# Performance work log

Measured on AMD Instinct MI355X. Metric: run time of the kernel, lower is better.

The kernel has to match this reference:

```python
import jax, jax.numpy as jnp
import numpy as np

B, S, HID = 1, 2048, 4096
NH, NKV, HD = 32, 8, 128
EPS = 1e-6
SCALE = HD ** -0.5


def _rope_cos_sin(seq_len, head_dim, base=1000000.0):
    inv_freq = 1.0 / (base ** (np.arange(0, head_dim, 2, dtype=np.float32) / head_dim))
    t = np.arange(seq_len, dtype=np.float32)
    freqs = np.outer(t, inv_freq)                      # [S, HD/2]
    emb = np.concatenate([freqs, freqs], axis=-1)       # [S, HD]
    return jnp.asarray(np.cos(emb))[None], jnp.asarray(np.sin(emb))[None]  # [1,S,HD]


def setup_inputs() -> dict:
    key = jax.random.key(0)
    ks = jax.random.split(key, 8)
    cos, sin = _rope_cos_sin(S, HD)
    inp = {
        "hidden_states": jax.random.normal(ks[0], (B, S, HID), jnp.float32),
        "cos": jnp.broadcast_to(cos, (B, S, HD)),
        "sin": jnp.broadcast_to(sin, (B, S, HD)),
        "Wq": jax.random.normal(ks[1], (NH * HD, HID), jnp.float32) * 0.02,
        "Wk": jax.random.normal(ks[2], (NKV * HD, HID), jnp.float32) * 0.02,
        "Wv": jax.random.normal(ks[3], (NKV * HD, HID), jnp.float32) * 0.02,
        "Wo": jax.random.normal(ks[4], (HID, NH * HD), jnp.float32) * 0.02,
        "q_norm_w": jnp.ones((HD,), jnp.float32),
        "k_norm_w": jnp.ones((HD,), jnp.float32),
    }
    return inp


def _rmsnorm(x, w, eps=EPS):
    var = jnp.mean(jnp.square(x), axis=-1, keepdims=True)
    return x * jax.lax.rsqrt(var + eps) * w


def _rotate_half(x):
    x1, x2 = jnp.split(x, 2, axis=-1)
    return jnp.concatenate([-x2, x1], axis=-1)


def _apply_rope(x, cos, sin):
    # x: [b,s,n,d]; cos/sin: [b,s,d] -> unsqueeze head dim (dim=2)
    c = cos[:, :, None, :]
    s = sin[:, :, None, :]
    return x * c + _rotate_half(x) * s


def reference(hidden_states, cos, sin, Wq, Wk, Wv, Wo, q_norm_w, k_norm_w):
    b, s, _ = hidden_states.shape
    q = (hidden_states @ Wq.T).reshape(b, s, NH, HD)
    k = (hidden_states @ Wk.T).reshape(b, s, NKV, HD)
    v = (hidden_states @ Wv.T).reshape(b, s, NKV, HD)
    # per-head RMSNorm on q and k
    q = _rmsnorm(q, q_norm_w)
    k = _rmsnorm(k, k_norm_w)
    # RoPE
    q = _apply_rope(q, cos, sin)
    k = _apply_rope(k, cos, sin)
    # GQA: expand kv heads to match query heads (group size = NH // NKV)
    g = NH // NKV
    k = jnp.repeat(k, g, axis=2)  # [b,s,NH,d]
    v = jnp.repeat(v, g, axis=2)
    # causal SDPA, layout bsnd
    scores = jnp.einsum("bqhd,bkhd->bhqk", q, k) * SCALE
    causal = jnp.tril(jnp.ones((s, s), dtype=bool))
    scores = jnp.where(causal[None, None], scores, jnp.finfo(scores.dtype).min)
    probs = jax.nn.softmax(scores, axis=-1)
    attn = jnp.einsum("bhqk,bkhd->bqhd", probs, v).reshape(b, s, NH * HD)
    return attn @ Wo.T
```

## Files before the change

### kernel.cpp

```cpp
#include <hip/hip_runtime.h>
#include <hip/hip_bf16.h>
#include <stdint.h>

#define S_LEN 2048
#define HIDD  4096
#define NH    32
#define NKV   8
#define HD    128
#define NQKV  6144
#define ATT_SCALE 0.08838834764831845f
#define LOG2E 1.4426950408889634f

typedef unsigned short u16;
typedef __attribute__((ext_vector_type(8))) short short8;
typedef __attribute__((ext_vector_type(4))) float f32x4;

__device__ __forceinline__ unsigned f2bfbits(float f){
  union{float f; unsigned u;} v; v.f = f;
  return (v.u + 0x7FFFu + ((v.u>>16)&1u)) >> 16;
}
__device__ __forceinline__ float bf2f(u16 b){
  union{unsigned u; float f;} v; v.u = ((unsigned)b)<<16;
  return v.f;
}
__device__ __forceinline__ unsigned packbf(float a, float b){
  return f2bfbits(a) | (f2bfbits(b)<<16);
}
__device__ __forceinline__ unsigned cvtpk(float lo, float hi){
  unsigned r;
  asm("v_cvt_pk_bf16_f32 %0, %1, %2" : "=v"(r) : "v"(lo), "v"(hi));
  return r;
}

#define GLOAD16(g, l) __builtin_amdgcn_global_load_lds( \
    (__attribute__((address_space(1))) void*)(g), \
    (__attribute__((address_space(3))) void*)(l), 16, 0, 0)

#define VMWAIT(n) asm volatile("s_waitcnt vmcnt(" #n ")" ::: "memory")
#define SCHED0() __builtin_amdgcn_sched_barrier(0)

__global__ __launch_bounds__(256) void cvt_all(const float* __restrict__ hs,
                                               const float* __restrict__ Wq,
                                               const float* __restrict__ Wk,
                                               const float* __restrict__ Wv,
                                               u16* __restrict__ Xb,
                                               u16* __restrict__ WQKV){
  const float* src; u16* dst; int n8;
  switch (blockIdx.y){
    case 0: src = hs; dst = Xb;                        n8 = S_LEN*HIDD/8;    break;
    case 1: src = Wq; dst = WQKV;                      n8 = NH*HD*HIDD/8;    break;
    case 2: src = Wk; dst = WQKV + (size_t)NH*HD*HIDD; n8 = NKV*HD*HIDD/8;   break;
    default:src = Wv; dst = WQKV + (size_t)(NH+NKV)*HD*HIDD; n8 = NKV*HD*HIDD/8; break;
  }
  int i = blockIdx.x*256 + threadIdx.x;
  if (i >= n8) return;
  const float4* p = (const float4*)src;
  float4 a = p[2*i], b = p[2*i+1];
  union { unsigned u[4]; short8 s; } o;
  o.u[0] = packbf(a.x, a.y); o.u[1] = packbf(a.z, a.w);
  o.u[2] = packbf(b.x, b.y); o.u[3] = packbf(b.z, b.w);
  *(short8*)(dst + (size_t)i*8) = o.s;
}

__global__ __launch_bounds__(256) void cvt_bf16(const float* __restrict__ in,
                                                u16* __restrict__ out, int n8){
  int i = blockIdx.x*256 + threadIdx.x;
  if (i >= n8) return;
  const float4* p = (const float4*)in;
  float4 a = p[2*i], b = p[2*i+1];
  union { unsigned u[4]; short8 s; } o;
  o.u[0] = packbf(a.x, a.y); o.u[1] = packbf(a.z, a.w);
  o.u[2] = packbf(b.x, b.y); o.u[3] = packbf(b.z, b.w);
  *(short8*)(out + (size_t)i*8) = o.s;
}

template<int BM, int BN, typename OT>
__global__ __launch_bounds__(512) void gemm_4ph(const u16* __restrict__ A,
                                                const u16* __restrict__ B,
                                                OT* __restrict__ C,
                                                int N, int K, int nbx){
  constexpr int MREP = BM/32;
  constexpr int NF   = BN/64;
  constexpr int AH   = BM/128;
  constexpr int ASZ  = BM*64;
  __shared__ __align__(16) char lds[4*ASZ + 65536];

  const int tid = threadIdx.x;
  const int w = tid>>6, lane = tid&63, ln = lane&15, g = lane>>4;
  const int wm = w>>2, wn = w&3;
  const int swz5 = ((ln>>3)&1)<<5;

  const int nwg = gridDim.x, flat = blockIdx.x;
  const int wg = (flat&7)*(nwg>>3) + (flat>>3);
  const int by = wg/nbx, bx = wg - by*nbx;
  const int m0 = by*BM, n0 = bx*BN;

  const int rs   = ((tid>>6)<<4) + ((tid&63)>>2);
  const int ksrc = ((tid&3)<<3) ^ (((tid>>5)&1)<<4);
  const u16* srcA[AH];
  #pragma unroll
  for (int h=0;h<AH;h++) srcA[h] = A + (size_t)(m0 + h*128 + rs)*K + ksrc;
  const u16* srcB[2];
  #pragma unroll
  for (int h=0;h<2;h++)  srcB[h] = B + (size_t)(n0 + h*128 + rs)*K + ksrc;

  #define AREG(bf,kh) (lds + ((bf)*2 + (kh))*ASZ)
  #define BREG(bf,kh) (lds + 4*ASZ + ((bf)*2 + (kh))*16384)

  #define STAGEPT(t, kh, bf) { const int off_ = (t)*64 + (kh)*32;                 \
    _Pragma("unroll") for (int h=0;h<AH;h++)                                      \
      GLOAD16(srcA[h]+off_, AREG(bf,kh) + h*8192 + w*1024);                       \
    _Pragma("unroll") for (int h=0;h<2;h++)                                       \
      GLOAD16(srcB[h]+off_, BREG(bf,kh) + h*8192 + w*1024); }

  f32x4 acc[MREP][NF];
  #pragma unroll
  for (int m=0;m<MREP;m++)
    #pragma unroll
    for (int n=0;n<NF;n++) acc[m][n] = (f32x4){0.f,0.f,0.f,0.f};
  short8 a0_[MREP], b0_[NF], a1_[MREP], b1_[NF];

  #define READ_SET(aset, bset, bf, kh) {                                          \
    _Pragma("unroll") for (int n=0;n<NF;n++)                                      \
      bset[n] = *(const short8*)(BREG(bf,kh) + (wn*NF+n)*1024 + ln*64 + ((g*16)^swz5)); \
    _Pragma("unroll") for (int m=0;m<MREP;m++)                                    \
      aset[m] = *(const short8*)(AREG(bf,kh) + (wm*MREP+m)*1024 + ln*64 + ((g*16)^swz5)); }
  #define MFMA_SET(aset, bset) { __builtin_amdgcn_s_setprio(1);                   \
    _Pragma("unroll") for (int m=0;m<MREP;m++)                                    \
      _Pragma("unroll") for (int n=0;n<NF;n++)                                    \
        acc[m][n] = __builtin_amdgcn_mfma_f32_16x16x32_bf16(aset[m], bset[n], acc[m][n], 0,0,0); \
    __builtin_amdgcn_s_setprio(0); }
  #define BARR() __builtin_amdgcn_s_barrier()
  #define VMST() do{ if constexpr (AH==2) { VMWAIT(4); } else { VMWAIT(3); } }while(0)

  STAGEPT(0,0,0); STAGEPT(0,1,0); STAGEPT(1,0,1);
  VMWAIT(0); BARR(); SCHED0();
  READ_SET(a0_, b0_, 0, 0);

  const int NIT = K>>7;
  #pragma unroll 1
  for (int it=0; it<NIT; ++it){
    const bool last = (it == NIT-1);
    const int t0 = 2*it;
    READ_SET(a1_, b1_, 0, 1);
    STAGEPT(t0+1, 1, 1);
    MFMA_SET(a0_, b0_);
    SCHED0(); VMST(); BARR(); SCHED0();
    READ_SET(a0_, b0_, 1, 0);
    if (!last) STAGEPT(t0+2, 0, 0);
    MFMA_SET(a1_, b1_);
    SCHED0(); if (last) { VMWAIT(0); } else { VMST(); } BARR(); SCHED0();
    READ_SET(a1_, b1_, 1, 1);
    if (!last) STAGEPT(t0+2, 1, 0);
    MFMA_SET(a0_, b0_);
    SCHED0(); if (!last) { VMST(); } BARR(); SCHED0();
    if (!last){ READ_SET(a0_, b0_, 0, 0); STAGEPT(t0+3, 0, 1); }
    MFMA_SET(a1_, b1_);
    if (!last){ SCHED0(); VMST(); BARR(); SCHED0(); }
  }

  #pragma unroll
  for (int mi=0; mi<MREP; mi++)
    #pragma unroll
    for (int n=0; n<NF; n++)
      #pragma unroll
      for (int r=0;r<4;r++){
        int row = m0 + (wm*MREP+mi)*16 + g*4 + r;
        int col = n0 + wn*(NF*16) + n*16 + ln;
        if constexpr (__is_same(OT, u16))
          C[(size_t)row*N + col] = (u16)f2bfbits(acc[mi][n][r]);
        else
          C[(size_t)row*N + col] = acc[mi][n][r];
      }
  #undef AREG
  #undef BREG
  #undef STAGEPT
  #undef READ_SET
  #undef MFMA_SET
  #undef BARR
  #undef VMST
}

__global__ __launch_bounds__(256) void norm_rope(const u16* __restrict__ QKVb,
                                                 const float* __restrict__ cosb,
                                                 const float* __restrict__ sinb,
                                                 const float* __restrict__ qw,
                                                 const float* __restrict__ kw,
                                                 u16* __restrict__ Qn,
                                                 u16* __restrict__ Kn,
                                                 u16* __restrict__ Vt){
  int w = threadIdx.x>>6, lane = threadIdx.x&63;
  int row = blockIdx.x*4 + w;
  int s = row / 48, slot = row - s*48;
  const u16* src = QKVb + (size_t)s*NQKV + slot*HD;
  float x0 = bf2f(src[lane]), x1 = bf2f(src[lane+64]);
  if (slot < 40){
    float ss = x0*x0 + x1*x1;
    #pragma unroll
    for (int off=1; off<64; off<<=1) ss += __shfl_xor(ss, off, 64);
    float r = rsqrtf(ss*(1.0f/128.0f) + 1e-6f);
    const float* wgt = (slot < 32) ? qw : kw;
    float y0 = x0*r*wgt[lane], y1 = x1*r*wgt[lane+64];
    float c0 = cosb[(size_t)s*HD+lane], c1 = cosb[(size_t)s*HD+lane+64];
    float s0 = sinb[(size_t)s*HD+lane], s1 = sinb[(size_t)s*HD+lane+64];
    float o0 = y0*c0 - y1*s0;
    float o1 = y1*c1 + y0*s1;
    float sc = (slot < 32) ? (ATT_SCALE*LOG2E) : 1.0f;
    u16* dst = (slot < 32) ? (Qn + ((size_t)slot*S_LEN + s)*HD)
                           : (Kn + ((size_t)(slot-32)*S_LEN + s)*HD);
    dst[lane]    = (u16)f2bfbits(o0*sc);
    dst[lane+64] = (u16)f2bfbits(o1*sc);
  } else {
    int kvh = slot - 40;
    u16* dst = Vt + (size_t)kvh*HD*S_LEN + s;
    dst[(size_t)lane*S_LEN]      = (u16)f2bfbits(x0);
    dst[(size_t)(lane+64)*S_LEN] = (u16)f2bfbits(x1);
  }
}

__global__ __launch_bounds__(256) void flash_attn(const u16* __restrict__ Qn,
                                                  const u16* __restrict__ Kn,
                                                  const u16* __restrict__ Vt,
                                                  u16* __restrict__ O){
  __shared__ u16 Ks[2][64*128];
  __shared__ u16 Vs[2][128*64];

  const int h = blockIdx.y;
  const int w = threadIdx.x>>6, lane = threadIdx.x&63, ln = lane&15, g = lane>>4;
  const int kvh = h>>2;
  const u16* Qh = Qn + (size_t)h*S_LEN*HD;
  const u16* Kh = Kn + (size_t)kvh*S_LEN*HD;
  const u16* Vh = Vt + (size_t)kvh*HD*S_LEN;

  const int krow_w = w*4 + g;
  const int ksw    = ((krow_w)&7)<<4;
  const int kcol   = ((ln*16) ^ ksw) >> 1;
  const int vrow_w = w*8 + (lane>>3);
  const int vsw    = ((lane>>3)&7)<<4;
  const int vcol   = (((lane&7)*16) ^ vsw) >> 1;

  #define STAGE_K(bufi, t) { \
    int kv0_ = (t)*64; \
    _Pragma("unroll") \
    for (int p=0;p<4;p++){ \
      const u16* ga = Kh + (size_t)(kv0_ + p*16 + krow_w)*HD + kcol; \
      GLOAD16(ga, (char*)&Ks[bufi][0] + p*4096 + w*1024); \
    } \
  }
  #define STAGE_V(bufi, t) { \
    int kv0_ = (t)*64; \
    _Pragma("unroll") \
    for (int p=0;p<4;p++){ \
      const u16* gv = Vh + (size_t)(p*32 + vrow_w)*S_LEN + kv0_ + vcol; \
      GLOAD16(gv, (char*)&Vs[bufi][0] + p*4096 + w*1024); \
    } \
  }
  #define QKT(dst, buf) { \
    _Pragma("unroll") for (int mt=0; mt<4; mt++){ \
      short8 kf[4]; \
      _Pragma("unroll") for (int c=0;c<4;c++) \
        kf[c] = *(const short8*)((const char*)&Ks[buf][0] \
                    + (mt*16+ln)*256 + ((c*64 + g*16) ^ ((ln&7)<<4))); \
      f32x4 qacc = (f32x4){0.f,0.f,0.f,0.f}; \
      __builtin_amdgcn_s_setprio(1); \
      _Pragma("unroll") for (int c=0;c<4;c++) \
        qacc = __builtin_amdgcn_mfma_f32_16x16x32_bf16(kf[c], qf[c], qacc, 0,0,0); \
      __builtin_amdgcn_s_setprio(0); \
      dst[mt] = qacc; \
    } }

  #define TILE_BODY(i, SC, SN) { \
    VMWAIT(0); \
    __builtin_amdgcn_s_barrier(); \
    if ((i)+1 < nt){ \
      QKT(SN, ((i)+1)&1); \
      if ((i)+2 < nt) STAGE_K(((i)+2)&1, (i)+2); \
      STAGE_V(((i)+1)&1, (i)+1); \
    } \
    const int kv0 = (i)*64; \
    float p[4][4]; \
    float mtile = -1e30f; \
    if ((i) < qb){ \
      _Pragma("unroll") for (int mt=0; mt<4; mt++) \
        _Pragma("unroll") for (int r=0;r<4;r++){ \
          p[mt][r] = SC[mt][r]; \
          mtile = fmaxf(mtile, SC[mt][r]); \
        } \
    } else { \
      _Pragma("unroll") for (int mt=0; mt<4; mt++) \
        _Pragma("unroll") for (int r=0;r<4;r++){ \
          int kv = kv0 + mt*16 + 4*g + r; \
          float sv = (kv <= qrow) ? SC[mt][r] : -1e30f; \
          p[mt][r] = sv; \
          mtile = fmaxf(mtile, sv); \
        } \
    } \
    mtile = fmaxf(mtile, __shfl_xor(mtile, 16, 64)); \
    mtile = fmaxf(mtile, __shfl_xor(mtile, 32, 64)); \
    bool defer = __all(mtile <= m_run + 11.5416f); \
    float m_new = defer ? m_run : fmaxf(m_run, mtile); \
    float l_tile = 0.f; \
    _Pragma("unroll") for (int mt=0; mt<4; mt++) \
      _Pragma("unroll") for (int r=0;r<4;r++){ \
        float e = exp2f(p[mt][r] - m_new); \
        p[mt][r] = e; \
        l_tile += e; \
      } \
    l_tile += __shfl_xor(l_tile, 16, 64); \
    l_tile += __shfl_xor(l_tile, 32, 64); \
    if (defer){ \
      l_run += l_tile; \
    } else { \
      float alpha = exp2f(m_run - m_new); \
      l_run = l_run*alpha + l_tile; \
      m_run = m_new; \
      _Pragma("unroll") for (int dt=0;dt<8;dt++) ot[dt] *= alpha; \
    } \
    short8 pf[2]; \
    _Pragma("unroll") for (int ks2=0; ks2<2; ks2++){ \
      unsigned pk00 = cvtpk(p[2*ks2  ][0], p[2*ks2  ][1]); \
      unsigned pk01 = cvtpk(p[2*ks2  ][2], p[2*ks2  ][3]); \
      unsigned pk10 = cvtpk(p[2*ks2+1][0], p[2*ks2+1][1]); \
      unsigned pk11 = cvtpk(p[2*ks2+1][2], p[2*ks2+1][3]); \
      int src0 = (((2*g  )&3)<<4) | ln; \
      int src1 = (((2*g+1)&3)<<4) | ln; \
      unsigned t00 = (unsigned)__shfl((int)pk00, src0, 64); \
      unsigned t10 = (unsigned)__shfl((int)pk10, src0, 64); \
      unsigned t01 = (unsigned)__shfl((int)pk01, src0, 64); \
      unsigned t11 = (unsigned)__shfl((int)pk11, src0, 64); \
      unsigned u00 = (unsigned)__shfl((int)pk00, src1, 64); \
      unsigned u10 = (unsigned)__shfl((int)pk10, src1, 64); \
      unsigned u01 = (unsigned)__shfl((int)pk01, src1, 64); \
      unsigned u11 = (unsigned)__shfl((int)pk11, src1, 64); \
      bool hiv = (g >= 2); \
      union { unsigned u[4]; short8 s; } pw; \
      pw.u[0] = hiv ? t10 : t00; \
      pw.u[1] = hiv ? t11 : t01; \
      pw.u[2] = hiv ? u10 : u00; \
      pw.u[3] = hiv ? u11 : u01; \
      pf[ks2] = pw.s; \
    } \
    _Pragma("unroll") for (int dt=0;dt<8;dt++){ \
      short8 vf[2]; \
      _Pragma("unroll") for (int ks2=0; ks2<2; ks2++) \
        vf[ks2] = *(const short8*)((const char*)&Vs[(i)&1][0] \
                    + (dt*16+ln)*128 + ((ks2*64 + g*16) ^ ((ln&7)<<4))); \
      __builtin_amdgcn_s_setprio(1); \
      _Pragma("unroll") for (int ks2=0; ks2<2; ks2++) \
        ot[dt] = __builtin_amdgcn_mfma_f32_16x16x32_bf16(vf[ks2], pf[ks2], ot[dt], 0,0,0); \
      __builtin_amdgcn_s_setprio(0); \
    } \
  }

  #pragma unroll 1
  for (int ph=0; ph<2; ph++){
    const int qb = ph ? (31 - blockIdx.x) : blockIdx.x;
    const int q0 = qb*64;
    const int qrow = q0 + w*16 + ln;

    short8 qf[4];
    #pragma unroll
    for (int c=0;c<4;c++)
      qf[c] = *(const short8*)(Qh + (size_t)qrow*HD + c*32 + g*8);

    f32x4 ot[8];
    #pragma unroll
    for (int dt=0;dt<8;dt++) ot[dt] = (f32x4){0.f,0.f,0.f,0.f};
    float m_run = -1e30f, l_run = 0.f;

    const int nt = qb + 1;

    STAGE_K(0, 0); STAGE_V(0, 0);
    if (nt > 1) STAGE_K(1, 1);
    VMWAIT(0);
    __builtin_amdgcn_s_barrier();

    f32x4 stA[4], stB[4];
    QKT(stA, 0);

    #pragma unroll 1
    for (int i=0; i<nt; i+=2){
      TILE_BODY(i, stA, stB);
      if (i+1 < nt) TILE_BODY(i+1, stB, stA);
    }
    __syncthreads();

    float inv = 1.0f / l_run;
    u16* orow = O + (size_t)qrow*(NH*HD) + h*HD;
    #pragma unroll
    for (int dt=0;dt<8;dt++){
      #pragma unroll
      for (int rr=0; rr<4; rr+=2){
        unsigned pkd = cvtpk(ot[dt][rr]*inv, ot[dt][rr+1]*inv);
        *(unsigned*)(orow + dt*16 + g*4 + rr) = pkd;
      }
    }
  }
  #undef STAGE_K
  #undef STAGE_V
  #undef QKT
  #undef TILE_BODY
}

extern "C" void kernel_launch(void* const* d_in, const int* in_sizes, int n_in,
                              void* d_out, int out_size, void* d_ws, size_t ws_size,
                              hipStream_t stream){
  (void)in_sizes; (void)n_in; (void)out_size; (void)ws_size;
  const float* hs   = (const float*)d_in[0];
  const float* cosb = (const float*)d_in[1];
  const float* sinb = (const float*)d_in[2];
  const float* Wq   = (const float*)d_in[3];
  const float* Wk   = (const float*)d_in[4];
  const float* Wv   = (const float*)d_in[5];
  const float* Wo   = (const float*)d_in[6];
  const float* qw   = (const float*)d_in[7];
  const float* kw   = (const float*)d_in[8];
  float* out = (float*)d_out;

  char* ws = (char*)d_ws;
  u16*   Xb    = (u16*)  (ws);
  u16*   WQKV  = (u16*)  (ws + 16777216);
  u16*   QKVb  = (u16*)  (ws + 67108864);
  u16*   attnB = (u16*)  (ws + 94371840);
  u16*   Qn    = (u16*)  (ws + 117440512);
  u16*   Kn    = (u16*)  (ws + 134217728);
  u16*   Vt    = (u16*)  (ws + 138412032);
  u16*   Wob   = WQKV;

  cvt_all<<<dim3(8192, 4), 256, 0, stream>>>(hs, Wq, Wk, Wv, Xb, WQKV);
  gemm_4ph<256,192,u16><<<256, 512, 0, stream>>>(Xb, WQKV, QKVb, NQKV, HIDD, NQKV/192);
  norm_rope<<<(S_LEN*48)/4, 256, 0, stream>>>(QKVb, cosb, sinb, qw, kw, Qn, Kn, Vt);
  cvt_bf16<<<(HIDD*NH*HD/8)/256, 256, 0, stream>>>(Wo, Wob, HIDD*NH*HD/8);
  flash_attn<<<dim3(16, NH), 256, 0, stream>>>(Qn, Kn, Vt, attnB);
  gemm_4ph<128,256,float><<<256, 512, 0, stream>>>(attnB, Wob, out, HIDD, HIDD, HIDD/256);
}
```

Baseline: 330.7 us.

## Restructure GEMM to 4-wave 256-thread blocks with smaller tiles and single register set

Both GEMMs now use 256-thread workgroups in a 2x2 wave layout. Tiles shrink to 128x192 for the QKV projection and 128x128 for the output projection, which doubles the grid to 512 blocks. The double-buffered register prefetch (two A/B operand sets) becomes a single set that is read right before each MFMA cluster, and the vmcnt wait counts are retuned for the new load counts. The aim is better CU occupancy and load balance across the GPU. In exchange, each block reuses data less and LDS read latency is no longer hidden behind the previous MFMA block.

```diff
diff --git a/kernel.cpp b/kernel.cpp
--- a/kernel.cpp
+++ b/kernel.cpp
@@ -75,19 +75,21 @@
 }
 
 template<int BM, int BN, typename OT>
-__global__ __launch_bounds__(512) void gemm_4ph(const u16* __restrict__ A,
+__global__ __launch_bounds__(256) void gemm_4ph(const u16* __restrict__ A,
                                                 const u16* __restrict__ B,
                                                 OT* __restrict__ C,
                                                 int N, int K, int nbx){
   constexpr int MREP = BM/32;
-  constexpr int NF   = BN/64;
-  constexpr int AH   = BM/128;
+  constexpr int NF   = BN/32;
+  constexpr int AL   = BM/64;
+  constexpr int BL   = BN/64;
   constexpr int ASZ  = BM*64;
-  __shared__ __align__(16) char lds[4*ASZ + 65536];
+  constexpr int BSZ  = BN*64;
+  __shared__ __align__(16) char lds[4*ASZ + 4*BSZ];
 
   const int tid = threadIdx.x;
   const int w = tid>>6, lane = tid&63, ln = lane&15, g = lane>>4;
-  const int wm = w>>2, wn = w&3;
+  const int wm = w>>1, wn = w&1;
   const int swz5 = ((ln>>3)&1)<<5;
 
   const int nwg = gridDim.x, flat = blockIdx.x;
@@ -97,66 +99,62 @@
 
   const int rs   = ((tid>>6)<<4) + ((tid&63)>>2);
   const int ksrc = ((tid&3)<<3) ^ (((tid>>5)&1)<<4);
-  const u16* srcA[AH];
+  const u16* srcA[AL];
   #pragma unroll
-  for (int h=0;h<AH;h++) srcA[h] = A + (size_t)(m0 + h*128 + rs)*K + ksrc;
-  const u16* srcB[2];
+  for (int j=0;j<AL;j++) srcA[j] = A + (size_t)(m0 + 64*j + rs)*K + ksrc;
+  const u16* srcB[BL];
   #pragma unroll
-  for (int h=0;h<2;h++)  srcB[h] = B + (size_t)(n0 + h*128 + rs)*K + ksrc;
+  for (int j=0;j<BL;j++) srcB[j] = B + (size_t)(n0 + 64*j + rs)*K + ksrc;
 
   #define AREG(bf,kh) (lds + ((bf)*2 + (kh))*ASZ)
-  #define BREG(bf,kh) (lds + 4*ASZ + ((bf)*2 + (kh))*16384)
+  #define BREG(bf,kh) (lds + 4*ASZ + ((bf)*2 + (kh))*BSZ)
 
   #define STAGEPT(t, kh, bf) { const int off_ = (t)*64 + (kh)*32;                 \
-    _Pragma("unroll") for (int h=0;h<AH;h++)                                      \
-      GLOAD16(srcA[h]+off_, AREG(bf,kh) + h*8192 + w*1024);                       \
-    _Pragma("unroll") for (int h=0;h<2;h++)                                       \
-      GLOAD16(srcB[h]+off_, BREG(bf,kh) + h*8192 + w*1024); }
+    _Pragma("unroll") for (int j=0;j<AL;j++)                                      \
+      GLOAD16(srcA[j]+off_, AREG(bf,kh) + (4*j+w)*1024);                          \
+    _Pragma("unroll") for (int j=0;j<BL;j++)                                      \
+      GLOAD16(srcB[j]+off_, BREG(bf,kh) + (4*j+w)*1024); }
 
   f32x4 acc[MREP][NF];
   #pragma unroll
   for (int m=0;m<MREP;m++)
     #pragma unroll
     for (int n=0;n<NF;n++) acc[m][n] = (f32x4){0.f,0.f,0.f,0.f};
-  short8 a0_[MREP], b0_[NF], a1_[MREP], b1_[NF];
-
-  #define READ_SET(aset, bset, bf, kh) {                                          \
-    _Pragma("unroll") for (int n=0;n<NF;n++)                                      \
-      bset[n] = *(const short8*)(BREG(bf,kh) + (wn*NF+n)*1024 + ln*64 + ((g*16)^swz5)); \
-    _Pragma("unroll") for (int m=0;m<MREP;m++)                                    \
-      aset[m] = *(const short8*)(AREG(bf,kh) + (wm*MREP+m)*1024 + ln*64 + ((g*16)^swz5)); }
-  #define MFMA_SET(aset, bset) { __builtin_amdgcn_s_setprio(1);                   \
+  short8 a_[MREP], b_[NF];
+
+  #define READA(bf,kh) { _Pragma("unroll") for (int m=0;m<MREP;m++)               \
+    a_[m] = *(const short8*)(AREG(bf,kh) + (wm*MREP+m)*1024 + ln*64 + ((g*16)^swz5)); }
+  #define READB(bf,kh) { _Pragma("unroll") for (int n=0;n<NF;n++)                 \
+    b_[n] = *(const short8*)(BREG(bf,kh) + (wn*NF+n)*1024 + ln*64 + ((g*16)^swz5)); }
+  #define MFMACLU() { __builtin_amdgcn_s_setprio(1);                              \
     _Pragma("unroll") for (int m=0;m<MREP;m++)                                    \
       _Pragma("unroll") for (int n=0;n<NF;n++)                                    \
-        acc[m][n] = __builtin_amdgcn_mfma_f32_16x16x32_bf16(aset[m], bset[n], acc[m][n], 0,0,0); \
+        acc[m][n] = __builtin_amdgcn_mfma_f32_16x16x32_bf16(a_[m], b_[n], acc[m][n], 0,0,0); \
     __builtin_amdgcn_s_setprio(0); }
   #define BARR() __builtin_amdgcn_s_barrier()
-  #define VMST() do{ if constexpr (AH==2) { VMWAIT(4); } else { VMWAIT(3); } }while(0)
+  #define VM2LP() do{ if constexpr (AL+BL==5) { VMWAIT(10); } else { VMWAIT(8); } }while(0)
+  #define VM1LP() do{ if constexpr (AL+BL==5) { VMWAIT(5); }  else { VMWAIT(4); } }while(0)
 
   STAGEPT(0,0,0); STAGEPT(0,1,0); STAGEPT(1,0,1);
   VMWAIT(0); BARR(); SCHED0();
-  READ_SET(a0_, b0_, 0, 0);
 
   const int NIT = K>>7;
   #pragma unroll 1
   for (int it=0; it<NIT; ++it){
     const bool last = (it == NIT-1);
     const int t0 = 2*it;
-    READ_SET(a1_, b1_, 0, 1);
-    STAGEPT(t0+1, 1, 1);
-    MFMA_SET(a0_, b0_);
-    SCHED0(); VMST(); BARR(); SCHED0();
-    READ_SET(a0_, b0_, 1, 0);
-    if (!last) STAGEPT(t0+2, 0, 0);
-    MFMA_SET(a1_, b1_);
-    SCHED0(); if (last) { VMWAIT(0); } else { VMST(); } BARR(); SCHED0();
-    READ_SET(a1_, b1_, 1, 1);
-    if (!last) STAGEPT(t0+2, 1, 0);
-    MFMA_SET(a0_, b0_);
-    SCHED0(); if (!last) { VMST(); } BARR(); SCHED0();
-    if (!last){ READ_SET(a0_, b0_, 0, 0); STAGEPT(t0+3, 0, 1); }
-    MFMA_SET(a1_, b1_);
-    if (!last){ SCHED0(); VMST(); BARR(); SCHED0(); }
+    READB(0,0); READA(0,0); STAGEPT(t0+1, 1, 1);
+    MFMACLU();
+    SCHED0(); VM2LP(); BARR(); SCHED0();
+    READB(0,1); READA(0,1); if (!last) STAGEPT(t0+2, 0, 0);
+    MFMACLU();
+    SCHED0(); if (last) { VM1LP(); } else { VM2LP(); } BARR(); SCHED0();
+    READB(1,0); READA(1,0); if (!last) STAGEPT(t0+2, 1, 0);
+    MFMACLU();
+    SCHED0(); if (last) { VMWAIT(0); } else { VM2LP(); } BARR(); SCHED0();
+    READB(1,1); READA(1,1); if (!last) STAGEPT(t0+3, 0, 1);
+    MFMACLU();
+    SCHED0(); if (!last) { VM2LP(); } BARR(); SCHED0();
   }
 
   #pragma unroll
@@ -166,7 +164,7 @@
       #pragma unroll
       for (int r=0;r<4;r++){
         int row = m0 + (wm*MREP+mi)*16 + g*4 + r;
-        int col = n0 + wn*(NF*16) + n*16 + ln;
+        int col = n0 + (wn*NF+n)*16 + ln;
         if constexpr (__is_same(OT, u16))
           C[(size_t)row*N + col] = (u16)f2bfbits(acc[mi][n][r]);
         else
@@ -175,10 +173,12 @@
   #undef AREG
   #undef BREG
   #undef STAGEPT
-  #undef READ_SET
-  #undef MFMA_SET
+  #undef READA
+  #undef READB
+  #undef MFMACLU
   #undef BARR
-  #undef VMST
+  #undef VM2LP
+  #undef VM1LP
 }
 
 __global__ __launch_bounds__(256) void norm_rope(const u16* __restrict__ QKVb,
@@ -428,9 +428,9 @@
   u16*   Wob   = WQKV;
 
   cvt_all<<<dim3(8192, 4), 256, 0, stream>>>(hs, Wq, Wk, Wv, Xb, WQKV);
-  gemm_4ph<256,192,u16><<<256, 512, 0, stream>>>(Xb, WQKV, QKVb, NQKV, HIDD, NQKV/192);
+  gemm_4ph<128,192,u16><<<512, 256, 0, stream>>>(Xb, WQKV, QKVb, NQKV, HIDD, NQKV/192);
   norm_rope<<<(S_LEN*48)/4, 256, 0, stream>>>(QKVb, cosb, sinb, qw, kw, Qn, Kn, Vt);
   cvt_bf16<<<(HIDD*NH*HD/8)/256, 256, 0, stream>>>(Wo, Wob, HIDD*NH*HD/8);
   flash_attn<<<dim3(16, NH), 256, 0, stream>>>(Qn, Kn, Vt, attnB);
-  gemm_4ph<128,256,float><<<256, 512, 0, stream>>>(attnB, Wob, out, HIDD, HIDD, HIDD/256);
-}
+  gemm_4ph<128,128,float><<<512, 256, 0, stream>>>(attnB, Wob, out, HIDD, HIDD, HIDD/128);
+}
```

After: 374.7 us. 1.13x slower.

## Fuse QK RMSNorm and RoPE into QKV GEMM epilogue, merge Wo conversion

Applied to the files above, without the earlier changes.

Replaces the QKV GEMM plus separate norm_rope kernel with a dedicated GEMM using 128x384 tiles, so each tile covers three whole heads. The epilogue stages the tile in LDS, then applies per-head RMSNorm, RoPE and the query scale, and writes Q, K and transposed V directly. This removes the intermediate QKV buffer round trip and one kernel launch. The Wo fp32-to-bf16 conversion is folded into cvt_all as a fifth grid row, which drops another launch. The new GEMM tile shape and its serial per-row epilogue (shuffle reductions, strided V-transpose stores) may be less efficient than the previous tuned GEMM configuration.

```diff
diff --git a/kernel.cpp b/kernel.cpp
--- a/kernel.cpp
+++ b/kernel.cpp
@@ -43,14 +43,17 @@
                                                const float* __restrict__ Wq,
                                                const float* __restrict__ Wk,
                                                const float* __restrict__ Wv,
+                                               const float* __restrict__ Wo,
                                                u16* __restrict__ Xb,
-                                               u16* __restrict__ WQKV){
+                                               u16* __restrict__ WQKV,
+                                               u16* __restrict__ Wob){
   const float* src; u16* dst; int n8;
   switch (blockIdx.y){
     case 0: src = hs; dst = Xb;                        n8 = S_LEN*HIDD/8;    break;
     case 1: src = Wq; dst = WQKV;                      n8 = NH*HD*HIDD/8;    break;
     case 2: src = Wk; dst = WQKV + (size_t)NH*HD*HIDD; n8 = NKV*HD*HIDD/8;   break;
-    default:src = Wv; dst = WQKV + (size_t)(NH+NKV)*HD*HIDD; n8 = NKV*HD*HIDD/8; break;
+    case 3: src = Wv; dst = WQKV + (size_t)(NH+NKV)*HD*HIDD; n8 = NKV*HD*HIDD/8; break;
+    default:src = Wo; dst = Wob;                       n8 = HIDD*NH*HD/8;    break;
   }
   int i = blockIdx.x*256 + threadIdx.x;
   if (i >= n8) return;
@@ -62,16 +65,142 @@
   *(short8*)(dst + (size_t)i*8) = o.s;
 }
 
-__global__ __launch_bounds__(256) void cvt_bf16(const float* __restrict__ in,
-                                                u16* __restrict__ out, int n8){
-  int i = blockIdx.x*256 + threadIdx.x;
-  if (i >= n8) return;
-  const float4* p = (const float4*)in;
-  float4 a = p[2*i], b = p[2*i+1];
-  union { unsigned u[4]; short8 s; } o;
-  o.u[0] = packbf(a.x, a.y); o.u[1] = packbf(a.z, a.w);
-  o.u[2] = packbf(b.x, b.y); o.u[3] = packbf(b.z, b.w);
-  *(short8*)(out + (size_t)i*8) = o.s;
+__global__ __launch_bounds__(512) void gemm1_fused(const u16* __restrict__ A,
+                                                   const u16* __restrict__ B,
+                                                   const float* __restrict__ cosb,
+                                                   const float* __restrict__ sinb,
+                                                   const float* __restrict__ qw,
+                                                   const float* __restrict__ kw,
+                                                   u16* __restrict__ Qn,
+                                                   u16* __restrict__ Kn,
+                                                   u16* __restrict__ Vt){
+  __shared__ __align__(16) char lds[131072];
+
+  const int tid = threadIdx.x;
+  const int w = tid>>6, lane = tid&63, ln = lane&15, g = lane>>4;
+  const int wm = w>>2, wn = w&3;
+  const int swz5 = ((ln>>3)&1)<<5;
+  const int K = HIDD;
+
+  const int nwg = gridDim.x, flat = blockIdx.x;
+  const int wg = (flat&7)*(nwg>>3) + (flat>>3);
+  const int by = wg>>4, bx = wg&15;
+  const int m0 = by*128, n0 = bx*384;
+
+  const int rs   = ((tid>>6)<<4) + ((tid&63)>>2);
+  const int ksrc = ((tid&3)<<3) ^ (((tid>>5)&1)<<4);
+  const u16* srcA0 = A + (size_t)(m0 + rs)*K + ksrc;
+  const u16* srcB[3];
+  #pragma unroll
+  for (int j=0;j<3;j++) srcB[j] = B + (size_t)(n0 + 128*j + rs)*K + ksrc;
+
+  #define G1_AREG(bf,kh) (lds + ((bf)*2 + (kh))*8192)
+  #define G1_BREG(bf,kh) (lds + 32768 + ((bf)*2 + (kh))*24576)
+
+  #define G1_STAGE(T, kh, bf) { const int off_ = (T)*64 + (kh)*32;                \
+    GLOAD16(srcA0 + off_, G1_AREG(bf,kh) + w*1024);                               \
+    _Pragma("unroll") for (int j=0;j<3;j++)                                       \
+      GLOAD16(srcB[j] + off_, G1_BREG(bf,kh) + j*8192 + w*1024); }
+
+  f32x4 acc[4][6];
+  #pragma unroll
+  for (int m=0;m<4;m++)
+    #pragma unroll
+    for (int n=0;n<6;n++) acc[m][n] = (f32x4){0.f,0.f,0.f,0.f};
+  short8 a_[4], b_[6];
+
+  #define G1_READA(bf,kh) { _Pragma("unroll") for (int m=0;m<4;m++)               \
+    a_[m] = *(const short8*)(G1_AREG(bf,kh) + (wm*4+m)*1024 + ln*64 + ((g*16)^swz5)); }
+  #define G1_READB(bf,kh) { _Pragma("unroll") for (int n=0;n<6;n++)               \
+    b_[n] = *(const short8*)(G1_BREG(bf,kh) + (wn*6+n)*1024 + ln*64 + ((g*16)^swz5)); }
+  #define G1_MFMA() { __builtin_amdgcn_s_setprio(1);                              \
+    _Pragma("unroll") for (int m=0;m<4;m++)                                       \
+      _Pragma("unroll") for (int n=0;n<6;n++)                                     \
+        acc[m][n] = __builtin_amdgcn_mfma_f32_16x16x32_bf16(a_[m], b_[n], acc[m][n], 0,0,0); \
+    __builtin_amdgcn_s_setprio(0); }
+  #define G1_BARR() __builtin_amdgcn_s_barrier()
+
+  G1_STAGE(0,0,0); G1_STAGE(0,1,0);
+  VMWAIT(4); G1_BARR(); SCHED0();
+
+  const int NT64 = K>>6;
+  #pragma unroll 1
+  for (int T=0; T<NT64; T+=2){
+    G1_READB(0,0); G1_READA(0,0); G1_STAGE(T+1, 0, 1);
+    G1_MFMA();
+    SCHED0(); VMWAIT(4); G1_BARR(); SCHED0();
+    G1_READB(0,1); G1_READA(0,1); G1_STAGE(T+1, 1, 1);
+    G1_MFMA();
+    SCHED0(); VMWAIT(4); G1_BARR(); SCHED0();
+    const bool s2 = (T+2) < NT64;
+    G1_READB(1,0); G1_READA(1,0); if (s2) G1_STAGE(T+2, 0, 0);
+    G1_MFMA();
+    SCHED0(); if (s2) { VMWAIT(4); } else { VMWAIT(0); } G1_BARR(); SCHED0();
+    G1_READB(1,1); G1_READA(1,1); if (s2) G1_STAGE(T+2, 1, 0);
+    G1_MFMA();
+    SCHED0(); if (s2) { VMWAIT(4); } else { VMWAIT(0); } G1_BARR(); SCHED0();
+  }
+
+  u16* clds = (u16*)lds;
+  #pragma unroll
+  for (int m=0;m<4;m++)
+    #pragma unroll
+    for (int n=0;n<6;n++)
+      #pragma unroll
+      for (int r=0;r<4;r++){
+        int row = wm*64 + m*16 + g*4 + r;
+        int col = wn*96 + n*16 + ln;
+        clds[row*384 + col] = (u16)f2bfbits(acc[m][n][r]);
+      }
+  G1_BARR();
+
+  const float wq0 = qw[lane], wq1 = qw[lane+64];
+  const float wk0 = kw[lane], wk1 = kw[lane+64];
+  const float qsc = ATT_SCALE*LOG2E;
+
+  #pragma unroll 1
+  for (int r8=0; r8<16; ++r8){
+    const int row = w*16 + r8;
+    const int s = m0 + row;
+    const float c0 = cosb[(size_t)s*HD + lane];
+    const float c1 = cosb[(size_t)s*HD + lane + 64];
+    const float s0 = sinb[(size_t)s*HD + lane];
+    const float s1 = sinb[(size_t)s*HD + lane + 64];
+    #pragma unroll
+    for (int lh=0; lh<3; ++lh){
+      const int slot = 3*bx + lh;
+      float x0 = bf2f(clds[row*384 + lh*128 + lane]);
+      float x1 = bf2f(clds[row*384 + lh*128 + lane + 64]);
+      if (slot < 40){
+        float ss = x0*x0 + x1*x1;
+        #pragma unroll
+        for (int off=1; off<64; off<<=1) ss += __shfl_xor(ss, off, 64);
+        float rr = rsqrtf(ss*(1.0f/128.0f) + 1e-6f);
+        bool isq = slot < 32;
+        float y0 = x0*rr*(isq ? wq0 : wk0);
+        float y1 = x1*rr*(isq ? wq1 : wk1);
+        float o0 = y0*c0 - y1*s0;
+        float o1 = y1*c1 + y0*s1;
+        float sc = isq ? qsc : 1.0f;
+        u16* dst = isq ? (Qn + ((size_t)slot*S_LEN + s)*HD)
+                       : (Kn + ((size_t)(slot-32)*S_LEN + s)*HD);
+        dst[lane]    = (u16)f2bfbits(o0*sc);
+        dst[lane+64] = (u16)f2bfbits(o1*sc);
+      } else {
+        int kvh = slot - 40;
+        u16* dst = Vt + (size_t)kvh*HD*S_LEN + s;
+        dst[(size_t)lane*S_LEN]      = (u16)f2bfbits(x0);
+        dst[(size_t)(lane+64)*S_LEN] = (u16)f2bfbits(x1);
+      }
+    }
+  }
+  #undef G1_AREG
+  #undef G1_BREG
+  #undef G1_STAGE
+  #undef G1_READA
+  #undef G1_READB
+  #undef G1_MFMA
+  #undef G1_BARR
 }
 
 template<int BM, int BN, typename OT>
@@ -179,43 +308,6 @@
   #undef MFMA_SET
   #undef BARR
   #undef VMST
-}
-
-__global__ __launch_bounds__(256) void norm_rope(const u16* __restrict__ QKVb,
-                                                 const float* __restrict__ cosb,
-                                                 const float* __restrict__ sinb,
-                                                 const float* __restrict__ qw,
-                                                 const float* __restrict__ kw,
-                                                 u16* __restrict__ Qn,
-                                                 u16* __restrict__ Kn,
-                                                 u16* __restrict__ Vt){
-  int w = threadIdx.x>>6, lane = threadIdx.x&63;
-  int row = blockIdx.x*4 + w;
-  int s = row / 48, slot = row - s*48;
-  const u16* src = QKVb + (size_t)s*NQKV + slot*HD;
-  float x0 = bf2f(src[lane]), x1 = bf2f(src[lane+64]);
-  if (slot < 40){
-    float ss = x0*x0 + x1*x1;
-    #pragma unroll
-    for (int off=1; off<64; off<<=1) ss += __shfl_xor(ss, off, 64);
-    float r = rsqrtf(ss*(1.0f/128.0f) + 1e-6f);
-    const float* wgt = (slot < 32) ? qw : kw;
-    float y0 = x0*r*wgt[lane], y1 = x1*r*wgt[lane+64];
-    float c0 = cosb[(size_t)s*HD+lane], c1 = cosb[(size_t)s*HD+lane+64];
-    float s0 = sinb[(size_t)s*HD+lane], s1 = sinb[(size_t)s*HD+lane+64];
-    float o0 = y0*c0 - y1*s0;
-    float o1 = y1*c1 + y0*s1;
-    float sc = (slot < 32) ? (ATT_SCALE*LOG2E) : 1.0f;
-    u16* dst = (slot < 32) ? (Qn + ((size_t)slot*S_LEN + s)*HD)
-                           : (Kn + ((size_t)(slot-32)*S_LEN + s)*HD);
-    dst[lane]    = (u16)f2bfbits(o0*sc);
-    dst[lane+64] = (u16)f2bfbits(o1*sc);
-  } else {
-    int kvh = slot - 40;
-    u16* dst = Vt + (size_t)kvh*HD*S_LEN + s;
-    dst[(size_t)lane*S_LEN]      = (u16)f2bfbits(x0);
-    dst[(size_t)(lane+64)*S_LEN] = (u16)f2bfbits(x1);
-  }
 }
 
 __global__ __launch_bounds__(256) void flash_attn(const u16* __restrict__ Qn,
@@ -418,19 +510,16 @@
   float* out = (float*)d_out;
 
   char* ws = (char*)d_ws;
-  u16*   Xb    = (u16*)  (ws);
-  u16*   WQKV  = (u16*)  (ws + 16777216);
-  u16*   QKVb  = (u16*)  (ws + 67108864);
-  u16*   attnB = (u16*)  (ws + 94371840);
-  u16*   Qn    = (u16*)  (ws + 117440512);
-  u16*   Kn    = (u16*)  (ws + 134217728);
-  u16*   Vt    = (u16*)  (ws + 138412032);
-  u16*   Wob   = WQKV;
-
-  cvt_all<<<dim3(8192, 4), 256, 0, stream>>>(hs, Wq, Wk, Wv, Xb, WQKV);
-  gemm_4ph<256,192,u16><<<256, 512, 0, stream>>>(Xb, WQKV, QKVb, NQKV, HIDD, NQKV/192);
-  norm_rope<<<(S_LEN*48)/4, 256, 0, stream>>>(QKVb, cosb, sinb, qw, kw, Qn, Kn, Vt);
-  cvt_bf16<<<(HIDD*NH*HD/8)/256, 256, 0, stream>>>(Wo, Wob, HIDD*NH*HD/8);
+  u16* Xb    = (u16*)(ws);
+  u16* WQKV  = (u16*)(ws + 16777216);
+  u16* Qn    = (u16*)(ws + 67108864);
+  u16* Kn    = (u16*)(ws + 83886080);
+  u16* Vt    = (u16*)(ws + 88080384);
+  u16* attnB = (u16*)(ws + 92274688);
+  u16* Wob   = (u16*)(ws + 109051904);
+
+  cvt_all<<<dim3(8192, 5), 256, 0, stream>>>(hs, Wq, Wk, Wv, Wo, Xb, WQKV, Wob);
+  gemm1_fused<<<256, 512, 0, stream>>>(Xb, WQKV, cosb, sinb, qw, kw, Qn, Kn, Vt);
   flash_attn<<<dim3(16, NH), 256, 0, stream>>>(Qn, Kn, Vt, attnB);
   gemm_4ph<128,256,float><<<256, 512, 0, stream>>>(attnB, Wob, out, HIDD, HIDD, HIDD/256);
 }
```

Result: no change. 336.0 us (+1.6%).
